# Performance work log

Measured on AMD Instinct MI355X. Metric: run time of the kernel, lower is better.

Reference implementation:

```python
import jax, jax.numpy as jnp
import numpy as np

# Graph: 3-node chain 0 -> 1 -> 2, node 0 takes the external stimulus.
B, T, CIN, H, W = 8, 8, 3, 64, 64
PROJ = 32            # proj_hidden_dim
CDIM = 32            # per-node cell input_dim (integrator output channels)
HID = 64             # per-node hidden_dim
NUM_NODE = 3
PROCESS_T = T + NUM_NODE - 1  # default process_time in forward


def _conv(x, w, b):
    # 3x3, stride 1, 'same' padding, NCHW / OIHW
    y = jax.lax.conv_general_dilated(x, w, (1, 1), ((1, 1), (1, 1)),
                                     dimension_numbers=('NCHW', 'OIHW', 'NCHW'))
    return y + b[None, :, None, None]


def _gru(x, h, wg, bg, wc, bc):
    # standard ConvGRU cell (topdown branch inactive: basal/apical dims = 0)
    gates = jax.nn.sigmoid(_conv(jnp.concatenate([x, h], axis=1), wg, bg))
    r, z = jnp.split(gates, 2, axis=1)
    cand = jnp.tanh(_conv(jnp.concatenate([x, r * h], axis=1), wc, bc))
    return z * h + (1.0 - z) * cand


def setup_inputs() -> dict:
    key = jax.random.key(0)
    ks = iter(jax.random.split(key, 40))

    def w(shape):
        fan_in = shape[1] * shape[2] * shape[3]
        return jax.random.normal(next(ks), shape, jnp.float32) / np.sqrt(fan_in)

    inp = {'x': jax.random.normal(next(ks), (B, T, CIN, H, W), jnp.float32)}
    # bottomup per-edge projection convs
    inp['Win0'] = w((PROJ, CIN, 3, 3)); inp['bin0'] = jnp.zeros((PROJ,), jnp.float32)
    inp['We10'] = w((PROJ, HID, 3, 3)); inp['be10'] = jnp.zeros((PROJ,), jnp.float32)
    inp['We21'] = w((PROJ, HID, 3, 3)); inp['be21'] = jnp.zeros((PROJ,), jnp.float32)
    # per-node integrator convs + ConvGRU cell params
    for n in range(NUM_NODE):
        inp[f'Wint{n}'] = w((CDIM, PROJ, 3, 3)); inp[f'bint{n}'] = jnp.zeros((CDIM,), jnp.float32)
        inp[f'Wg{n}'] = w((2 * HID, CDIM + HID, 3, 3)); inp[f'bg{n}'] = jnp.zeros((2 * HID,), jnp.float32)
        inp[f'Wc{n}'] = w((HID, CDIM + HID, 3, 3)); inp[f'bc{n}'] = jnp.zeros((HID,), jnp.float32)
    return inp


def reference(x, Win0, bin0, We10, be10, We21, be21,
              Wint0, bint0, Wg0, bg0, Wc0, bc0,
              Wint1, bint1, Wg1, bg1, Wc1, bc1,
              Wint2, bint2, Wg2, bg2, Wc2, bc2):
    h = [jnp.zeros((B, HID, H, W), x.dtype) for _ in range(NUM_NODE)]
    h_prev = list(h)
    for t in range(PROCESS_T):
        new_h = list(h)
        # node 0: external stimulus (zeros after seq ends), becomes active at t=0
        inp = x[:, t] if t < T else jnp.zeros_like(x[:, 0])
        bu0 = _conv(_conv(inp, Win0, bin0), Wint0, bint0)
        new_h[0] = _gru(bu0, h[0], Wg0, bg0, Wc0, bc0)
        # node 1: in-edge from node 0, activates at t=1 (wave propagation)
        if t >= 1:
            bu1 = _conv(_conv(h_prev[0], We10, be10), Wint1, bint1)
            new_h[1] = _gru(bu1, h[1], Wg1, bg1, Wc1, bc1)
        # node 2: in-edge from node 1, activates at t=2
        if t >= 2:
            bu2 = _conv(_conv(h_prev[1], We21, be21), Wint2, bint2)
            new_h[2] = _gru(bu2, h[2], Wg2, bg2, Wc2, bc2)
        h = new_h
        h_prev = list(h)
    # output node index 2
    return h[2]
```

## Files before the change

kernel.cpp:

```cpp
#include <hip/hip_runtime.h>
#include <hip/hip_bf16.h>

#define BATCH 8
#define TSEQ 8
#define HH 64
#define WW 64
#define HID 64
#define PT 10

typedef __bf16 bf16_t;
typedef __bf16 bf16x8 __attribute__((ext_vector_type(8)));
typedef float  f32x4  __attribute__((ext_vector_type(4)));

__device__ __forceinline__ float fsigmoid(float v) {
    float e = __builtin_amdgcn_exp2f(-1.4426950408889634f * v);
    return __builtin_amdgcn_rcpf(1.0f + e);
}
__device__ __forceinline__ float ftanh(float v) {
    float e = __builtin_amdgcn_exp2f(2.8853900817779268f * v);
    return 1.0f - 2.0f * __builtin_amdgcn_rcpf(1.0f + e);
}

struct PackSeg { const float* src; bf16_t* dst; int NT16; int KC; int CinReal; int begin; };
struct PackArgs { PackSeg s[12]; int total; };

__global__ void wpack_all(PackArgs P) {
    int idx = blockIdx.x * 256 + threadIdx.x;
    if (idx >= P.total) return;
    int si = 0;
#pragma unroll
    for (int i = 1; i < 12; ++i) if (idx >= P.s[i].begin) si = i;
    PackSeg sg = P.s[si];
    int l = idx - sg.begin;
    int j    = l & 7;
    int lane = (l >> 3) & 63;
    int rest = l >> 9;
    int nt   = rest % sg.NT16;
    int chunk = rest / sg.NT16;
    int kc  = chunk % sg.KC;
    int tap = chunk / sg.KC;
    int co = nt * 16 + (lane & 15);
    int ci = kc * 32 + (lane >> 4) * 8 + j;
    float v = (ci < sg.CinReal) ? sg.src[((long)co * sg.CinReal + ci) * 9 + tap] : 0.0f;
    sg.dst[l] = (bf16_t)v;
}

__global__ void xcvt_k(const float* __restrict__ x, bf16_t* __restrict__ xb) {
    int idx = blockIdx.x * 256 + threadIdx.x;
    if (idx >= 8 * 8 * 64 * 64 * 64) return;
    int c  = idx & 63;
    int xx = (idx >> 6) & 63;
    int y  = (idx >> 12) & 63;
    int b  = (idx >> 18) & 7;
    int t  = idx >> 21;
    float v = 0.0f;
    if (c < 3) v = x[((((long)b * TSEQ + t) * 3 + c) * 64 + y) * 64 + xx];
    xb[idx] = (bf16_t)v;
}

__global__ void hout_k(const float* __restrict__ hf, float* __restrict__ out) {
    int idx = blockIdx.x * 256 + threadIdx.x;
    if (idx >= 8 * 64 * 64 * 64) return;
    int xx = idx & 63;
    int y  = (idx >> 6) & 63;
    int c  = (idx >> 12) & 63;
    int b  = idx >> 18;
    out[idx] = hf[((((long)b * 64 + y) * 64 + xx) * 64) + c];
}

struct NP {
    const bf16_t* A0;
    const bf16_t* A1;
    const float*  Zf;
    const float*  Hf;
    const bf16_t* Hb;
    const bf16_t* Wp;
    const float*  bias;
    bf16_t* outB;
    float*  outF;
};
struct NPs { NP n[3]; };

template <int CIN0, int CIN1, int COUT, int MODE, int MINW>
__global__ __launch_bounds__(256, MINW) void mconv(NPs P)
{
    constexpr int CIN  = CIN0 + CIN1;
    constexpr int NT16 = COUT / 16;
    constexpr int NCH  = CIN / 8;
    constexpr int KC   = CIN / 32;
    constexpr int NCHUNK = 9 * KC;
    constexpr int PSB  = CIN * 2 + 8;
    constexpr int NT_W = (NT16 > 4) ? NT16 / 4 : 1;
    constexpr int NW_N = NT16 / NT_W;
    constexpr int NW_M = 4 / NW_N;
    constexpr int MT_W = 8 / NW_M;
    constexpr int PF   = 4;
    constexpr int ASMEM = 4 * 66 * PSB;
    constexpr int OSB   = COUT + 8;
    constexpr int OSMEM = (MODE == 0) ? 128 * OSB * 2
                                      : 128 * 68 * 4 + 128 * 72 * 2;
    constexpr int SMEM  = (ASMEM > OSMEM) ? ASMEM : OSMEM;

    const NP np   = P.n[blockIdx.y];
    const int tid  = threadIdx.x;
    const int lane = tid & 63;
    const int w    = tid >> 6;
    const int b  = blockIdx.x & 7;
    const int y0 = (blockIdx.x >> 3) * 2;

    __shared__ __align__(16) char smem[SMEM];

    const int nt0 = (w % NW_N) * NT_W;
    const int mt0 = (w / NW_N) * MT_W;
    const int l15 = lane & 15;
    const int kg  = lane >> 4;

    const bf16_t* wp0 = np.Wp + (size_t)nt0 * 512 + (size_t)lane * 8;
    bf16x8 ring[PF][NT_W];
#pragma unroll
    for (int i = 0; i < PF; ++i)
#pragma unroll
        for (int ni = 0; ni < NT_W; ++ni)
            ring[i][ni] = *(const bf16x8*)(wp0 + (size_t)i * (NT16 * 512) + ni * 512);

    for (int c = tid; c < 4 * 66 * NCH; c += 256) {
        int ry = c / (66 * NCH);
        int r  = c - ry * 66 * NCH;
        int px = r / NCH;
        int c2 = r - px * NCH;
        int gy = y0 + ry - 1, gx = px - 1;
        bf16x8 v = {};
        if ((unsigned)gy < 64u && (unsigned)gx < 64u) {
            long pix = ((long)b * 64 + gy) * 64 + gx;
            int ci = c2 * 8;
            if (CIN1 == 0 || ci < CIN0) v = *(const bf16x8*)(np.A0 + pix * CIN0 + ci);
            else                        v = *(const bf16x8*)(np.A1 + pix * CIN1 + (ci - CIN0));
        }
        *(bf16x8*)(smem + (ry * 66 + px) * PSB + c2 * 16) = v;
    }
    __syncthreads();

    int ab[3];
#pragma unroll
    for (int kx = 0; kx < 3; ++kx)
        ab[kx] = (l15 + kx) * PSB + kg * 16;

    f32x4 acc[MT_W][NT_W];
#pragma unroll
    for (int mi = 0; mi < MT_W; ++mi)
#pragma unroll
        for (int ni = 0; ni < NT_W; ++ni) {
            float bv = np.bias[(nt0 + ni) * 16 + l15];
            acc[mi][ni] = (f32x4){bv, bv, bv, bv};
        }

#pragma unroll
    for (int ch = 0; ch < NCHUNK; ++ch) {
        const int tap = ch / KC, kc = ch % KC;
        const int ky = tap / 3, kx = tap % 3;
        bf16x8 bcur[NT_W];
#pragma unroll
        for (int ni = 0; ni < NT_W; ++ni) bcur[ni] = ring[ch % PF][ni];
        if (ch + PF < NCHUNK) {
#pragma unroll
            for (int ni = 0; ni < NT_W; ++ni)
                ring[ch % PF][ni] =
                    *(const bf16x8*)(wp0 + (size_t)(ch + PF) * (NT16 * 512) + ni * 512);
        }
#pragma unroll
        for (int mi = 0; mi < MT_W; ++mi) {
            const int mt = mt0 + mi;
            const int row = mt >> 2, xseg = mt & 3;
            const int imm = (row + ky) * (66 * PSB) + xseg * (16 * PSB) + kc * 64;
            bf16x8 a = *(const bf16x8*)(smem + ab[kx] + imm);
#pragma unroll
            for (int ni = 0; ni < NT_W; ++ni)
                acc[mi][ni] = __builtin_amdgcn_mfma_f32_16x16x32_bf16(
                    a, bcur[ni], acc[mi][ni], 0, 0, 0);
        }
    }

    __syncthreads();
    const long pixbase = ((long)b * 64 + y0) * 64;

    if (MODE == 0) {
        bf16_t* so = (bf16_t*)smem;
#pragma unroll
        for (int mi = 0; mi < MT_W; ++mi) {
            const int mt = mt0 + mi;
            const int lpx0 = (mt >> 2) * 64 + (mt & 3) * 16 + kg * 4;
#pragma unroll
            for (int ni = 0; ni < NT_W; ++ni) {
                const int co = (nt0 + ni) * 16 + l15;
#pragma unroll
                for (int reg = 0; reg < 4; ++reg)
                    so[(lpx0 + reg) * OSB + co] = (bf16_t)acc[mi][ni][reg];
            }
        }
        __syncthreads();
        for (int i = tid; i < 128 * (COUT / 8); i += 256) {
            const int p = i / (COUT / 8);
            const int cc = (i % (COUT / 8)) * 8;
            *(bf16x8*)(np.outB + (pixbase + p) * COUT + cc) =
                *(const bf16x8*)(so + p * OSB + cc);
        }
    } else if (MODE == 1) {
        bf16_t* srh = (bf16_t*)smem;
        float*  sz  = (float*)(smem + 128 * 72 * 2);
#pragma unroll
        for (int mi = 0; mi < MT_W; ++mi) {
            const int mt = mt0 + mi;
            const int lpx0 = (mt >> 2) * 64 + (mt & 3) * 16 + kg * 4;
#pragma unroll
            for (int ni = 0; ni < NT_W; ++ni) {
                const int co = (nt0 + ni) * 16 + l15;
#pragma unroll
                for (int reg = 0; reg < 4; ++reg) {
                    const int lpx = lpx0 + reg;
                    float s = fsigmoid(acc[mi][ni][reg]);
                    if (co < HID) {
                        float hv = (float)np.Hb[(pixbase + lpx) * HID + co];
                        srh[lpx * 72 + co] = (bf16_t)(s * hv);
                    } else {
                        sz[lpx * 68 + (co - HID)] = s;
                    }
                }
            }
        }
        __syncthreads();
        for (int i = tid; i < 128 * 8; i += 256) {
            const int p = i >> 3, cc = (i & 7) * 8;
            *(bf16x8*)(np.outB + (pixbase + p) * HID + cc) =
                *(const bf16x8*)(srh + p * 72 + cc);
        }
        for (int i = tid; i < 128 * 16; i += 256) {
            const int p = i >> 4, cc = (i & 15) * 4;
            *(f32x4*)(np.outF + (pixbase + p) * HID + cc) =
                *(const f32x4*)(sz + p * 68 + cc);
        }
    } else {
        float*  shf = (float*)smem;
        bf16_t* shb = (bf16_t*)(smem + 128 * 68 * 4);
#pragma unroll
        for (int mi = 0; mi < MT_W; ++mi) {
            const int mt = mt0 + mi;
            const int lpx0 = (mt >> 2) * 64 + (mt & 3) * 16 + kg * 4;
#pragma unroll
            for (int ni = 0; ni < NT_W; ++ni) {
                const int co = (nt0 + ni) * 16 + l15;
#pragma unroll
                for (int reg = 0; reg < 4; ++reg) {
                    const int lpx = lpx0 + reg;
                    float cd = ftanh(acc[mi][ni][reg]);
                    float z  = np.Zf[(pixbase + lpx) * HID + co];
                    float ho = np.Hf[(pixbase + lpx) * HID + co];
                    float hn = z * ho + (1.0f - z) * cd;
                    shf[lpx * 68 + co] = hn;
                    shb[lpx * 72 + co] = (bf16_t)hn;
                }
            }
        }
        __syncthreads();
        for (int i = tid; i < 128 * 16; i += 256) {
            const int p = i >> 4, cc = (i & 15) * 4;
            *(f32x4*)(np.outF + (pixbase + p) * HID + cc) =
                *(const f32x4*)(shf + p * 68 + cc);
        }
        for (int i = tid; i < 128 * 8; i += 256) {
            const int p = i >> 3, cc = (i & 7) * 8;
            *(bf16x8*)(np.outB + (pixbase + p) * HID + cc) =
                *(const bf16x8*)(shb + p * 72 + cc);
        }
    }
}

extern "C" void kernel_launch(void* const* d_in, const int* in_sizes, int n_in,
                              void* d_out, int out_size, void* d_ws, size_t ws_size,
                              hipStream_t stream) {
    const float* x    = (const float*)d_in[0];
    const float* Win0 = (const float*)d_in[1];
    const float* bin0 = (const float*)d_in[2];
    const float* We10 = (const float*)d_in[3];
    const float* be10 = (const float*)d_in[4];
    const float* We21 = (const float*)d_in[5];
    const float* be21 = (const float*)d_in[6];
    const float* Wint[3] = {(const float*)d_in[7],  (const float*)d_in[13], (const float*)d_in[19]};
    const float* bint[3] = {(const float*)d_in[8],  (const float*)d_in[14], (const float*)d_in[20]};
    const float* Wg[3]   = {(const float*)d_in[9],  (const float*)d_in[15], (const float*)d_in[21]};
    const float* bg[3]   = {(const float*)d_in[10], (const float*)d_in[16], (const float*)d_in[22]};
    const float* Wc[3]   = {(const float*)d_in[11], (const float*)d_in[17], (const float*)d_in[23]};
    const float* bc[3]   = {(const float*)d_in[12], (const float*)d_in[18], (const float*)d_in[24]};
    (void)in_sizes; (void)n_in; (void)out_size; (void)ws_size;

    const long PIX  = (long)BATCH * HH * WW;
    const size_t HFSZ = (size_t)PIX * HID * 4;
    const size_t HBSZ = (size_t)PIX * HID * 2;
    const long PSZ  = PIX * 32;
    const long RHSZ = PIX * HID;
    const long ZSZ  = PIX * HID;

    char* wsb = (char*)d_ws;
    size_t off = 0;
    auto alloc = [&](size_t bytes) -> char* {
        char* q = wsb + off;
        off = (off + bytes + 255) & ~(size_t)255;
        return q;
    };

    float*  hF[6]; bf16_t* hB[6];
    hF[0] = (float*)alloc(HFSZ); hF[1] = (float*)alloc(HFSZ); hF[2] = (float*)alloc(HFSZ);
    hB[0] = (bf16_t*)alloc(HBSZ); hB[1] = (bf16_t*)alloc(HBSZ); hB[2] = (bf16_t*)alloc(HBSZ);
    const size_t zeroBytes = 3 * HFSZ + 3 * HBSZ;
    hF[3] = (float*)alloc(HFSZ); hF[4] = (float*)alloc(HFSZ); hF[5] = (float*)alloc(HFSZ);
    hB[3] = (bf16_t*)alloc(HBSZ); hB[4] = (bf16_t*)alloc(HBSZ); hB[5] = (bf16_t*)alloc(HBSZ);
    bf16_t* xb = (bf16_t*)alloc((size_t)TSEQ * PIX * 64 * 2);
    bf16_t* p  = (bf16_t*)alloc((size_t)3 * PSZ * 2);
    bf16_t* bu = (bf16_t*)alloc((size_t)3 * PSZ * 2);
    bf16_t* rh = (bf16_t*)alloc((size_t)3 * RHSZ * 2);
    float*  zb = (float*) alloc((size_t)3 * ZSZ * 4);
    bf16_t* WpIn0 = (bf16_t*)alloc((size_t)18432 * 2);
    bf16_t* WpE10 = (bf16_t*)alloc((size_t)18432 * 2);
    bf16_t* WpE21 = (bf16_t*)alloc((size_t)18432 * 2);
    bf16_t* WpInt[3], *WpG[3], *WpC[3];
    for (int n = 0; n < 3; ++n) WpInt[n] = (bf16_t*)alloc((size_t)9216 * 2);
    for (int n = 0; n < 3; ++n) WpG[n]   = (bf16_t*)alloc((size_t)110592 * 2);
    for (int n = 0; n < 3; ++n) WpC[n]   = (bf16_t*)alloc((size_t)55296 * 2);

    hipMemsetAsync(hF[0], 0, zeroBytes, stream);

    PackArgs PA{};
    int beg = 0;
    auto seg = [&](int i, const float* src, bf16_t* dst, int Cout, int CinPad, int CinReal) {
        PA.s[i] = {src, dst, Cout / 16, CinPad / 32, CinReal, beg};
        beg += 9 * (CinPad / 32) * (Cout / 16) * 512;
    };
    seg(0, Win0, WpIn0, 32, 64, 3);
    seg(1, We10, WpE10, 32, 64, 64);
    seg(2, We21, WpE21, 32, 64, 64);
    for (int n = 0; n < 3; ++n) seg(3 + n, Wint[n], WpInt[n], 32, 32, 32);
    for (int n = 0; n < 3; ++n) seg(6 + n, Wg[n],   WpG[n],   128, 96, 96);
    for (int n = 0; n < 3; ++n) seg(9 + n, Wc[n],   WpC[n],   64, 96, 96);
    PA.total = beg;
    wpack_all<<<(PA.total + 255) / 256, 256, 0, stream>>>(PA);
    xcvt_k<<<(8 * 8 * 64 * 64 * 64 + 255) / 256, 256, 0, stream>>>(x, xb);

    float*  hFc[3] = {hF[0], hF[1], hF[2]};
    float*  hFn[3] = {hF[3], hF[4], hF[5]};
    bf16_t* hBc[3] = {hB[0], hB[1], hB[2]};
    bf16_t* hBn[3] = {hB[3], hB[4], hB[5]};
    const bf16_t* WpE[2] = {WpE10, WpE21};
    const float*  beE[2] = {be10, be21};

    const dim3 T(256);
    const int GX = BATCH * (HH / 2);

    for (int t = 0; t < PT; ++t) {
        const int nLo = (t > 7) ? (t - 7) : 0;
        const int nHi = (t < 2) ? t : 2;
        const int nAct = nHi - nLo + 1;
        {
            NPs P{};
            for (int i = 0; i < nAct; ++i) {
                int n = nLo + i;
                if (n == 0) {
                    P.n[i].A0 = xb + (long)t * PIX * 64;
                    P.n[i].Wp = WpIn0; P.n[i].bias = bin0;
                } else {
                    P.n[i].A0 = hBc[n - 1];
                    P.n[i].Wp = WpE[n - 1]; P.n[i].bias = beE[n - 1];
                }
                P.n[i].outB = p + (long)n * PSZ;
            }
            mconv<64, 0, 32, 0, 3><<<dim3(GX, nAct), T, 0, stream>>>(P);
        }
        {
            NPs P{};
            for (int i = 0; i < nAct; ++i) {
                int n = nLo + i;
                P.n[i].A0 = p + (long)n * PSZ;
                P.n[i].Wp = WpInt[n]; P.n[i].bias = bint[n];
                P.n[i].outB = bu + (long)n * PSZ;
            }
            mconv<32, 0, 32, 0, 4><<<dim3(GX, nAct), T, 0, stream>>>(P);
        }
        {
            NPs P{};
            for (int i = 0; i < nAct; ++i) {
                int n = nLo + i;
                P.n[i].A0 = bu + (long)n * PSZ; P.n[i].A1 = hBc[n]; P.n[i].Hb = hBc[n];
                P.n[i].Wp = WpG[n]; P.n[i].bias = bg[n];
                P.n[i].outB = rh + (long)n * RHSZ; P.n[i].outF = zb + (long)n * ZSZ;
            }
            mconv<32, 64, 128, 1, 3><<<dim3(GX, nAct), T, 0, stream>>>(P);
        }
        {
            NPs P{};
            for (int i = 0; i < nAct; ++i) {
                int n = nLo + i;
                P.n[i].A0 = bu + (long)n * PSZ; P.n[i].A1 = rh + (long)n * RHSZ;
                P.n[i].Zf = zb + (long)n * ZSZ; P.n[i].Hf = hFc[n];
                P.n[i].Wp = WpC[n]; P.n[i].bias = bc[n];
                P.n[i].outB = hBn[n]; P.n[i].outF = hFn[n];
            }
            mconv<32, 64, 64, 2, 3><<<dim3(GX, nAct), T, 0, stream>>>(P);
        }
        for (int n = nLo; n <= nHi; ++n) {
            float* tf = hFc[n]; hFc[n] = hFn[n]; hFn[n] = tf;
            bf16_t* tb = hBc[n]; hBc[n] = hBn[n]; hBn[n] = tb;
        }
    }

    hout_k<<<(8 * 64 * 64 * 64 + 255) / 256, 256, 0, stream>>>(hFc[2], (float*)d_out);
}
```

Measured before the change: 764.4 us.

## Fuse projection and integrator convs, batch node-0 input path, fuse output transpose

```diff
diff --git a/kernel.cpp b/kernel.cpp
--- a/kernel.cpp
+++ b/kernel.cpp
@@ -7,6 +7,7 @@
 #define WW 64
 #define HID 64
 #define PT 10
+#define PIXN 32768
 
 typedef __bf16 bf16_t;
 typedef __bf16 bf16x8 __attribute__((ext_vector_type(8)));
@@ -58,14 +59,137 @@
     xb[idx] = (bf16_t)v;
 }
 
-__global__ void hout_k(const float* __restrict__ hf, float* __restrict__ out) {
-    int idx = blockIdx.x * 256 + threadIdx.x;
-    if (idx >= 8 * 64 * 64 * 64) return;
-    int xx = idx & 63;
-    int y  = (idx >> 6) & 63;
-    int c  = (idx >> 12) & 63;
-    int b  = idx >> 18;
-    out[idx] = hf[((((long)b * 64 + y) * 64 + xx) * 64) + c];
+struct PJ {
+    const bf16_t* X;
+    const bf16_t* Wpj;
+    const float*  bpj;
+    const bf16_t* Wit;
+    const float*  bit;
+    bf16_t* outB;
+};
+struct PJs { PJ u[8]; };
+
+__global__ __launch_bounds__(256, 2) void projint_k(PJs P) {
+    constexpr int PSBX = 136;
+    constexpr int PSBP = 72;
+    constexpr int POFF = 6 * 66 * PSBX;
+    __shared__ __align__(16) char smem[6 * 66 * PSBX + 4 * 66 * PSBP];
+
+    const PJ u = P.u[blockIdx.y];
+    const int tid = threadIdx.x, lane = tid & 63, w = tid >> 6;
+    const int b = blockIdx.x & 7, y0 = (blockIdx.x >> 3) * 2;
+    const int l15 = lane & 15, kg = lane >> 4;
+
+    const bf16_t* wpp = u.Wpj + (size_t)(w & 1) * 512 + (size_t)lane * 8;
+    bf16x8 ring[4];
+#pragma unroll
+    for (int i = 0; i < 4; ++i) ring[i] = *(const bf16x8*)(wpp + (size_t)i * 1024);
+
+    for (int c = tid; c < 6 * 66 * 8; c += 256) {
+        int ry = c / (66 * 8);
+        int r  = c - ry * (66 * 8);
+        int px = r >> 3, c2 = r & 7;
+        int gy = y0 + ry - 2, gx = px - 1;
+        bf16x8 v = {};
+        if ((unsigned)gy < 64u && (unsigned)gx < 64u)
+            v = *(const bf16x8*)(u.X + (((long)b * 64 + gy) * 64 + gx) * 64 + c2 * 8);
+        *(bf16x8*)(smem + (ry * 66 + px) * PSBX + c2 * 16) = v;
+    }
+    if (tid < 32) {
+        int row = tid >> 3;
+        int col = ((tid >> 2) & 1) ? 65 : 0;
+        int chk = tid & 3;
+        *(bf16x8*)(smem + POFF + (row * 66 + col) * PSBP + chk * 16) = (bf16x8){};
+    }
+    if (y0 == 0)
+        for (int i = tid; i < 66 * 4; i += 256)
+            *(bf16x8*)(smem + POFF + (0 * 66 + (i >> 2)) * PSBP + (i & 3) * 16) = (bf16x8){};
+    if (y0 == 62)
+        for (int i = tid; i < 66 * 4; i += 256)
+            *(bf16x8*)(smem + POFF + (3 * 66 + (i >> 2)) * PSBP + (i & 3) * 16) = (bf16x8){};
+    __syncthreads();
+
+    const int ntp = w & 1, mtb = (w >> 1) * 8;
+    f32x4 pacc[8];
+    {
+        float bv = u.bpj[ntp * 16 + l15];
+#pragma unroll
+        for (int mi = 0; mi < 8; ++mi) pacc[mi] = (f32x4){bv, bv, bv, bv};
+    }
+#pragma unroll
+    for (int ch = 0; ch < 18; ++ch) {
+        const int tap = ch >> 1, kc = ch & 1;
+        const int ky = tap / 3, kx = tap % 3;
+        bf16x8 bcur = ring[ch & 3];
+        if (ch + 4 < 18) ring[ch & 3] = *(const bf16x8*)(wpp + (size_t)(ch + 4) * 1024);
+#pragma unroll
+        for (int mi = 0; mi < 8; ++mi) {
+            const int mt = mtb + mi;
+            const int prow = mt >> 2, xseg = mt & 3;
+            const int addr = ((prow + ky) * 66 + xseg * 16 + l15 + kx) * PSBX
+                           + kg * 16 + kc * 64;
+            bf16x8 a = *(const bf16x8*)(smem + addr);
+            pacc[mi] = __builtin_amdgcn_mfma_f32_16x16x32_bf16(a, bcur, pacc[mi], 0, 0, 0);
+        }
+    }
+    const bf16_t* wpi = u.Wit + (size_t)(w & 1) * 512 + (size_t)lane * 8;
+    bf16x8 ring2[4];
+#pragma unroll
+    for (int i = 0; i < 4; ++i) ring2[i] = *(const bf16x8*)(wpi + (size_t)i * 1024);
+#pragma unroll
+    for (int mi = 0; mi < 8; ++mi) {
+        const int mt = mtb + mi;
+        const int prow = mt >> 2, xseg = mt & 3;
+        const int gyp = y0 - 1 + prow;
+        if (gyp >= 0 && gyp < 64) {
+            const int co = ntp * 16 + l15;
+#pragma unroll
+            for (int reg = 0; reg < 4; ++reg) {
+                const int pxi = xseg * 16 + kg * 4 + reg;
+                *(bf16_t*)(smem + POFF + (prow * 66 + pxi + 1) * PSBP + co * 2) =
+                    (bf16_t)pacc[mi][reg];
+            }
+        }
+    }
+    __syncthreads();
+
+    const int nti = w & 1, mtb2 = (w >> 1) * 4;
+    f32x4 iacc[4];
+    {
+        float bv = u.bit[nti * 16 + l15];
+#pragma unroll
+        for (int mi = 0; mi < 4; ++mi) iacc[mi] = (f32x4){bv, bv, bv, bv};
+    }
+#pragma unroll
+    for (int ch = 0; ch < 9; ++ch) {
+        const int ky = ch / 3, kx = ch % 3;
+        bf16x8 bcur = ring2[ch & 3];
+        if (ch + 4 < 9) ring2[ch & 3] = *(const bf16x8*)(wpi + (size_t)(ch + 4) * 1024);
+#pragma unroll
+        for (int mi = 0; mi < 4; ++mi) {
+            const int mt = mtb2 + mi;
+            const int r2 = mt >> 2, xseg = mt & 3;
+            const int addr = POFF + ((r2 + ky) * 66 + xseg * 16 + l15 + kx) * PSBP + kg * 16;
+            bf16x8 a = *(const bf16x8*)(smem + addr);
+            iacc[mi] = __builtin_amdgcn_mfma_f32_16x16x32_bf16(a, bcur, iacc[mi], 0, 0, 0);
+        }
+    }
+    bf16_t* so = (bf16_t*)smem;
+#pragma unroll
+    for (int mi = 0; mi < 4; ++mi) {
+        const int mt = mtb2 + mi;
+        const int lpx0 = (mt >> 2) * 64 + (mt & 3) * 16 + kg * 4;
+        const int co = nti * 16 + l15;
+#pragma unroll
+        for (int reg = 0; reg < 4; ++reg)
+            so[(lpx0 + reg) * 40 + co] = (bf16_t)iacc[mi][reg];
+    }
+    __syncthreads();
+    const long pixbase = ((long)b * 64 + y0) * 64;
+    for (int i = tid; i < 128 * 4; i += 256) {
+        const int p = i >> 2, cc = (i & 3) * 8;
+        *(bf16x8*)(u.outB + (pixbase + p) * 32 + cc) = *(const bf16x8*)(so + p * 40 + cc);
+    }
 }
 
 struct NP {
@@ -96,9 +220,8 @@
     constexpr int MT_W = 8 / NW_M;
     constexpr int PF   = 4;
     constexpr int ASMEM = 4 * 66 * PSB;
-    constexpr int OSB   = COUT + 8;
-    constexpr int OSMEM = (MODE == 0) ? 128 * OSB * 2
-                                      : 128 * 68 * 4 + 128 * 72 * 2;
+    constexpr int OSMEM = (MODE == 1 || MODE == 2) ? 128 * 68 * 4 + 128 * 72 * 2
+                                                   : 128 * 69 * 4;
     constexpr int SMEM  = (ASMEM > OSMEM) ? ASMEM : OSMEM;
 
     const NP np   = P.n[blockIdx.y];
@@ -183,28 +306,7 @@
     __syncthreads();
     const long pixbase = ((long)b * 64 + y0) * 64;
 
-    if (MODE == 0) {
-        bf16_t* so = (bf16_t*)smem;
-#pragma unroll
-        for (int mi = 0; mi < MT_W; ++mi) {
-            const int mt = mt0 + mi;
-            const int lpx0 = (mt >> 2) * 64 + (mt & 3) * 16 + kg * 4;
-#pragma unroll
-            for (int ni = 0; ni < NT_W; ++ni) {
-                const int co = (nt0 + ni) * 16 + l15;
-#pragma unroll
-                for (int reg = 0; reg < 4; ++reg)
-                    so[(lpx0 + reg) * OSB + co] = (bf16_t)acc[mi][ni][reg];
-            }
-        }
-        __syncthreads();
-        for (int i = tid; i < 128 * (COUT / 8); i += 256) {
-            const int p = i / (COUT / 8);
-            const int cc = (i % (COUT / 8)) * 8;
-            *(bf16x8*)(np.outB + (pixbase + p) * COUT + cc) =
-                *(const bf16x8*)(so + p * OSB + cc);
-        }
-    } else if (MODE == 1) {
+    if (MODE == 1) {
         bf16_t* srh = (bf16_t*)smem;
         float*  sz  = (float*)(smem + 128 * 72 * 2);
 #pragma unroll
@@ -238,7 +340,7 @@
             *(f32x4*)(np.outF + (pixbase + p) * HID + cc) =
                 *(const f32x4*)(sz + p * 68 + cc);
         }
-    } else {
+    } else if (MODE == 2) {
         float*  shf = (float*)smem;
         bf16_t* shb = (bf16_t*)(smem + 128 * 68 * 4);
 #pragma unroll
@@ -270,6 +372,36 @@
             const int p = i >> 3, cc = (i & 7) * 8;
             *(bf16x8*)(np.outB + (pixbase + p) * HID + cc) =
                 *(const bf16x8*)(shb + p * 72 + cc);
+        }
+    } else {
+        float* shf = (float*)smem;
+#pragma unroll
+        for (int mi = 0; mi < MT_W; ++mi) {
+            const int mt = mt0 + mi;
+            const int lpx0 = (mt >> 2) * 64 + (mt & 3) * 16 + kg * 4;
+#pragma unroll
+            for (int ni = 0; ni < NT_W; ++ni) {
+                const int co = (nt0 + ni) * 16 + l15;
+#pragma unroll
+                for (int reg = 0; reg < 4; ++reg) {
+                    const int lpx = lpx0 + reg;
+                    float cd = ftanh(acc[mi][ni][reg]);
+                    float z  = np.Zf[(pixbase + lpx) * HID + co];
+                    float ho = np.Hf[(pixbase + lpx) * HID + co];
+                    shf[lpx * 69 + co] = z * ho + (1.0f - z) * cd;
+                }
+            }
+        }
+        __syncthreads();
+        for (int i = tid; i < 128 * 16; i += 256) {
+            const int j = i >> 4;
+            const int cc = (i & 15) * 4;
+            const int co = j & 63, yr = j >> 6;
+            f32x4 v = { shf[(yr * 64 + cc + 0) * 69 + co],
+                        shf[(yr * 64 + cc + 1) * 69 + co],
+                        shf[(yr * 64 + cc + 2) * 69 + co],
+                        shf[(yr * 64 + cc + 3) * 69 + co] };
+            *(f32x4*)(np.outF + (((long)b * 64 + co) * 64 + (y0 + yr)) * 64 + cc) = v;
         }
     }
 }
@@ -292,7 +424,7 @@
     const float* bc[3]   = {(const float*)d_in[12], (const float*)d_in[18], (const float*)d_in[24]};
     (void)in_sizes; (void)n_in; (void)out_size; (void)ws_size;
 
-    const long PIX  = (long)BATCH * HH * WW;
+    const long PIX  = (long)PIXN;
     const size_t HFSZ = (size_t)PIX * HID * 4;
     const size_t HBSZ = (size_t)PIX * HID * 2;
     const long PSZ  = PIX * 32;
@@ -313,11 +445,11 @@
     const size_t zeroBytes = 3 * HFSZ + 3 * HBSZ;
     hF[3] = (float*)alloc(HFSZ); hF[4] = (float*)alloc(HFSZ); hF[5] = (float*)alloc(HFSZ);
     hB[3] = (bf16_t*)alloc(HBSZ); hB[4] = (bf16_t*)alloc(HBSZ); hB[5] = (bf16_t*)alloc(HBSZ);
-    bf16_t* xb = (bf16_t*)alloc((size_t)TSEQ * PIX * 64 * 2);
-    bf16_t* p  = (bf16_t*)alloc((size_t)3 * PSZ * 2);
-    bf16_t* bu = (bf16_t*)alloc((size_t)3 * PSZ * 2);
-    bf16_t* rh = (bf16_t*)alloc((size_t)3 * RHSZ * 2);
-    float*  zb = (float*) alloc((size_t)3 * ZSZ * 4);
+    bf16_t* xb  = (bf16_t*)alloc((size_t)TSEQ * PIX * 64 * 2);
+    bf16_t* bu0 = (bf16_t*)alloc((size_t)TSEQ * PSZ * 2);
+    bf16_t* bu  = (bf16_t*)alloc((size_t)3 * PSZ * 2);
+    bf16_t* rh  = (bf16_t*)alloc((size_t)3 * RHSZ * 2);
+    float*  zb  = (float*) alloc((size_t)3 * ZSZ * 4);
     bf16_t* WpIn0 = (bf16_t*)alloc((size_t)18432 * 2);
     bf16_t* WpE10 = (bf16_t*)alloc((size_t)18432 * 2);
     bf16_t* WpE21 = (bf16_t*)alloc((size_t)18432 * 2);
@@ -344,6 +476,17 @@
     wpack_all<<<(PA.total + 255) / 256, 256, 0, stream>>>(PA);
     xcvt_k<<<(8 * 8 * 64 * 64 * 64 + 255) / 256, 256, 0, stream>>>(x, xb);
 
+    {
+        PJs PJ{};
+        for (int t = 0; t < TSEQ; ++t) {
+            PJ.u[t].X = xb + (long)t * PIX * 64;
+            PJ.u[t].Wpj = WpIn0; PJ.u[t].bpj = bin0;
+            PJ.u[t].Wit = WpInt[0]; PJ.u[t].bit = bint[0];
+            PJ.u[t].outB = bu0 + (long)t * PSZ;
+        }
+        projint_k<<<dim3(256, TSEQ), dim3(256), 0, stream>>>(PJ);
+    }
+
     float*  hFc[3] = {hF[0], hF[1], hF[2]};
     float*  hFn[3] = {hF[3], hF[4], hF[5]};
     bf16_t* hBc[3] = {hB[0], hB[1], hB[2]};
@@ -352,63 +495,63 @@
     const float*  beE[2] = {be10, be21};
 
     const dim3 T(256);
-    const int GX = BATCH * (HH / 2);
+    const int GX = 256;
 
     for (int t = 0; t < PT; ++t) {
         const int nLo = (t > 7) ? (t - 7) : 0;
         const int nHi = (t < 2) ? t : 2;
         const int nAct = nHi - nLo + 1;
+
+        if (t >= 1) {
+            const int lo = (nLo > 1) ? nLo : 1;
+            const int cnt = nHi - lo + 1;
+            if (cnt > 0) {
+                PJs PJ{};
+                for (int i = 0; i < cnt; ++i) {
+                    int n = lo + i;
+                    PJ.u[i].X = hBc[n - 1];
+                    PJ.u[i].Wpj = WpE[n - 1]; PJ.u[i].bpj = beE[n - 1];
+                    PJ.u[i].Wit = WpInt[n];   PJ.u[i].bit = bint[n];
+                    PJ.u[i].outB = bu + (long)n * PSZ;
+                }
+                projint_k<<<dim3(GX, cnt), T, 0, stream>>>(PJ);
+            }
+        }
         {
             NPs P{};
             for (int i = 0; i < nAct; ++i) {
                 int n = nLo + i;
-                if (n == 0) {
-                    P.n[i].A0 = xb + (long)t * PIX * 64;
-                    P.n[i].Wp = WpIn0; P.n[i].bias = bin0;
-                } else {
-                    P.n[i].A0 = hBc[n - 1];
-                    P.n[i].Wp = WpE[n - 1]; P.n[i].bias = beE[n - 1];
-                }
-                P.n[i].outB = p + (long)n * PSZ;
-            }
-            mconv<64, 0, 32, 0, 3><<<dim3(GX, nAct), T, 0, stream>>>(P);
-        }
-        {
+                P.n[i].A0 = (n == 0) ? (bu0 + (long)t * PSZ) : (bu + (long)n * PSZ);
+                P.n[i].A1 = hBc[n]; P.n[i].Hb = hBc[n];
+                P.n[i].Wp = WpG[n]; P.n[i].bias = bg[n];
+                P.n[i].outB = rh + (long)n * RHSZ; P.n[i].outF = zb + (long)n * ZSZ;
+            }
+            mconv<32, 64, 128, 1, 3><<<dim3(GX, nAct), T, 0, stream>>>(P);
+        }
+        if (t < PT - 1) {
             NPs P{};
             for (int i = 0; i < nAct; ++i) {
                 int n = nLo + i;
-                P.n[i].A0 = p + (long)n * PSZ;
-                P.n[i].Wp = WpInt[n]; P.n[i].bias = bint[n];
-                P.n[i].outB = bu + (long)n * PSZ;
-            }
-            mconv<32, 0, 32, 0, 4><<<dim3(GX, nAct), T, 0, stream>>>(P);
-        }
-        {
-            NPs P{};
-            for (int i = 0; i < nAct; ++i) {
-                int n = nLo + i;
-                P.n[i].A0 = bu + (long)n * PSZ; P.n[i].A1 = hBc[n]; P.n[i].Hb = hBc[n];
-                P.n[i].Wp = WpG[n]; P.n[i].bias = bg[n];
-                P.n[i].outB = rh + (long)n * RHSZ; P.n[i].outF = zb + (long)n * ZSZ;
-            }
-            mconv<32, 64, 128, 1, 3><<<dim3(GX, nAct), T, 0, stream>>>(P);
-        }
-        {
-            NPs P{};
-            for (int i = 0; i < nAct; ++i) {
-                int n = nLo + i;
-                P.n[i].A0 = bu + (long)n * PSZ; P.n[i].A1 = rh + (long)n * RHSZ;
+                P.n[i].A0 = (n == 0) ? (bu0 + (long)t * PSZ) : (bu + (long)n * PSZ);
+                P.n[i].A1 = rh + (long)n * RHSZ;
                 P.n[i].Zf = zb + (long)n * ZSZ; P.n[i].Hf = hFc[n];
                 P.n[i].Wp = WpC[n]; P.n[i].bias = bc[n];
                 P.n[i].outB = hBn[n]; P.n[i].outF = hFn[n];
             }
             mconv<32, 64, 64, 2, 3><<<dim3(GX, nAct), T, 0, stream>>>(P);
+        } else {
+            NPs P{};
+            P.n[0].A0 = bu + (long)2 * PSZ;
+            P.n[0].A1 = rh + (long)2 * RHSZ;
+            P.n[0].Zf = zb + (long)2 * ZSZ; P.n[0].Hf = hFc[2];
+            P.n[0].Wp = WpC[2]; P.n[0].bias = bc[2];
+            P.n[0].outF = (float*)d_out;
+            mconv<32, 64, 64, 3, 3><<<dim3(GX, 1), T, 0, stream>>>(P);
         }
         for (int n = nLo; n <= nHi; ++n) {
+            if (t == PT - 1) break;
             float* tf = hFc[n]; hFc[n] = hFn[n]; hFn[n] = tf;
             bf16_t* tb = hBc[n]; hBc[n] = hBn[n]; hBn[n] = tb;
         }
     }
-
-    hout_k<<<(8 * 64 * 64 * 64 + 255) / 256, 256, 0, stream>>>(hFc[2], (float*)d_out);
-}
+}
```

Result: no change. 762.1 us (-0.3%).
